# Performance work log

Hardware: AMD Instinct MI355X
Metric: run time of the kernel (lower is better)

## Reference

```python
import jax, jax.numpy as jnp
import numpy as np
import math

B, S, HID, NH = 4, 2048, 1024, 16
HD = HID // NH  # head dim = 64


def setup_inputs() -> dict:
    key = jax.random.key(0)
    ks = jax.random.split(key, 8)
    sc = 0.02
    return {
        "x": jax.random.normal(ks[0], (B, S, HID), dtype=jnp.float32),
        "att_mask": jnp.zeros((B, 1, 1, S), dtype=jnp.float32),
        "Wq": jax.random.normal(ks[1], (HID, HID), dtype=jnp.float32) * sc,
        "bq": jax.random.normal(ks[2], (HID,), dtype=jnp.float32) * sc,
        "Wk": jax.random.normal(ks[3], (HID, HID), dtype=jnp.float32) * sc,
        "bk": jax.random.normal(ks[4], (HID,), dtype=jnp.float32) * sc,
        "Wv": jax.random.normal(ks[5], (HID, HID), dtype=jnp.float32) * sc,
        "bv": jax.random.normal(ks[6], (HID,), dtype=jnp.float32) * sc,
    }


def reference(x, att_mask, Wq, bq, Wk, bk, Wv, bv):
    # quant_mode=False path: QuantLinear acts as a plain affine projection
    # (the running min/max stats only calibrate `scale`, which is unused in
    # the float path), and IntSoftmax reduces to a standard softmax.
    q = x @ Wq.T + bq  # [B,S,HID]
    k = x @ Wk.T + bk
    v = x @ Wv.T + bv
    # split heads: [B,S,HID] -> [B,NH,S,HD]
    q = q.reshape(B, S, NH, HD).transpose(0, 2, 1, 3)
    k = k.reshape(B, S, NH, HD).transpose(0, 2, 1, 3)
    v = v.reshape(B, S, NH, HD).transpose(0, 2, 1, 3)
    scores = jnp.einsum("bhqd,bhkd->bhqk", q, k) / math.sqrt(HD) + att_mask
    probs = jax.nn.softmax(scores, axis=-1)  # [B,NH,S,S]
    ctx = jnp.einsum("bhqk,bhkd->bhqd", probs, v)  # [B,NH,S,HD]
    return ctx.transpose(0, 2, 1, 3).reshape(B, S, HID)
```

## Files before the change

kernel.cpp:

```cpp
#include <hip/hip_runtime.h>
#include <hip/hip_bf16.h>
#include <cstdint>
#include <cstddef>

#define BB   4
#define SS   2048
#define HIDD 1024
#define NHH  16
#define HDD  64
#define MM   (BB*SS)
#define L2E  1.4426950408889634f
#define SH4  5.770780163555854f

typedef __bf16    bf16x8 __attribute__((ext_vector_type(8)));
typedef float     f32x4  __attribute__((ext_vector_type(4)));
typedef _Float16  half4  __attribute__((ext_vector_type(4)));
typedef _Float16  half8  __attribute__((ext_vector_type(8)));
typedef _Float16  half2v __attribute__((ext_vector_type(2)));

__device__ __forceinline__ unsigned short f2b(float f) {
    unsigned u = __builtin_bit_cast(unsigned, f);
    return (unsigned short)((u + 0x7FFFu + ((u >> 16) & 1u)) >> 16);
}

__device__ __forceinline__ half2v pkrtz(float a, float b) {
    return __builtin_bit_cast(half2v, __builtin_amdgcn_cvt_pkrtz(a, b));
}

__device__ __forceinline__ void gl_lds16(const void* g, void* l) {
    __builtin_amdgcn_global_load_lds(
        (const __attribute__((address_space(1))) void*)g,
        (__attribute__((address_space(3))) void*)l, 16, 0, 0);
}

#define NX4 (MM * HIDD / 4)
#define NW4 (HIDD * HIDD / 4)
__global__ __launch_bounds__(256) void cvt_all(
    const float* __restrict__ x,  const float* __restrict__ wq,
    const float* __restrict__ wk, const float* __restrict__ wv,
    unsigned short* __restrict__ xb, unsigned short* __restrict__ wb)
{
    int i = blockIdx.x * 256 + threadIdx.x;
    const float* src; unsigned short* dst; int off;
    if (i < NX4) { src = x; dst = xb; off = i; }
    else {
        int j = i - NX4;
        int w = j >> 18;
        off = j & (NW4 - 1);
        src = (w == 0) ? wq : (w == 1) ? wk : wv;
        dst = wb + (size_t)w * HIDD * HIDD;
    }
    float4 v = reinterpret_cast<const float4*>(src)[off];
    ushort4 o;
    o.x = f2b(v.x); o.y = f2b(v.y); o.z = f2b(v.z); o.w = f2b(v.w);
    reinterpret_cast<ushort4*>(dst)[off] = o;
}

__global__ __launch_bounds__(256, 3) void qkv_gemm(
    const unsigned short* __restrict__ xb,
    const unsigned short* __restrict__ wb,
    const float* __restrict__ bq, const float* __restrict__ bk, const float* __restrict__ bv,
    unsigned short* __restrict__ Qb, unsigned short* __restrict__ Kb,
    _Float16* __restrict__ Vtb)
{
    __shared__ unsigned short lA[128 * 64];
    __shared__ unsigned short lB[128 * 64];

    const int tid  = threadIdx.x;
    const int wave = tid >> 6, lane = tid & 63;
    const int lh   = lane & 15, quad = lane >> 4;
    const int l7   = lh & 7;
    const int m0   = blockIdx.x * 128;
    const int opn  = blockIdx.y;
    const int op   = opn >> 3;
    const int n0   = (opn & 7) * 128;
    const unsigned short* W = wb + (size_t)op * HIDD * HIDD;
    const float* bias = (op == 0) ? bq : (op == 1) ? bk : bv;

    f32x4 acc[4][4];
#pragma unroll
    for (int i = 0; i < 4; i++)
#pragma unroll
        for (int j = 0; j < 4; j++) acc[i][j] = f32x4{0.f, 0.f, 0.f, 0.f};

    const int wm = wave & 1, wn = wave >> 1;
    const unsigned short* srcA = (op == 2) ? lA : lB;
    const unsigned short* srcB = (op == 2) ? lB : lA;
    const int offA = (op == 2) ? wm : wn;
    const int offB = (op == 2) ? wn : wm;

    const int srow = tid >> 3;
    const int sg   = tid & 7;

    for (int k0 = 0; k0 < HIDD; k0 += 64) {
#pragma unroll
        for (int rr = 0; rr < 4; rr++) {
            const int row = srow + rr * 32;
            const int gcol = k0 + ((sg ^ (row & 7)) << 3);
            gl_lds16(&xb[(size_t)(m0 + row) * HIDD + gcol], &lA[row * 64 + sg * 8]);
            gl_lds16(&W [(size_t)(n0 + row) * HIDD + gcol], &lB[row * 64 + sg * 8]);
        }
        __syncthreads();

#pragma unroll
        for (int kk = 0; kk < 2; kk++) {
            bf16x8 aF[4], bF[4];
#pragma unroll
            for (int i = 0; i < 4; i++) {
                const int row = offA * 64 + i * 16 + lh;
                aF[i] = *reinterpret_cast<const bf16x8*>(
                    &srcA[row * 64 + (((kk * 4 + quad) ^ l7) << 3)]);
            }
#pragma unroll
            for (int j = 0; j < 4; j++) {
                const int row = offB * 64 + j * 16 + lh;
                bF[j] = *reinterpret_cast<const bf16x8*>(
                    &srcB[row * 64 + (((kk * 4 + quad) ^ l7) << 3)]);
            }
#pragma unroll
            for (int i = 0; i < 4; i++)
#pragma unroll
                for (int j = 0; j < 4; j++)
                    acc[i][j] = __builtin_amdgcn_mfma_f32_16x16x32_bf16(aF[i], bF[j], acc[i][j], 0, 0, 0);
        }
        __syncthreads();
    }

    if (op == 2) {
#pragma unroll
        for (int j = 0; j < 4; j++) {
            const int n = n0 + offB * 64 + j * 16 + lh;
            const float bvv = bias[n];
            const int h = n >> 6, d = n & 63;
#pragma unroll
            for (int i = 0; i < 4; i++) {
                const int mrow = m0 + offA * 64 + i * 16 + quad * 4;
                const int b_ = mrow >> 11, s_ = mrow & 2047;
                half2v h01 = pkrtz(acc[i][j][0] + bvv, acc[i][j][1] + bvv);
                half2v h23 = pkrtz(acc[i][j][2] + bvv, acc[i][j][3] + bvv);
                half4 hv; hv[0] = h01[0]; hv[1] = h01[1]; hv[2] = h23[0]; hv[3] = h23[1];
                size_t a = ((size_t)(b_ * NHH + h) * HDD + d) * SS + s_;
                *reinterpret_cast<half4*>(&Vtb[a]) = hv;
            }
        }
    } else {
        const float qs = (op == 0) ? (0.125f * L2E) : 1.0f;
        unsigned short* dst = (op == 0) ? Qb : Kb;
#pragma unroll
        for (int i = 0; i < 4; i++) {
            const int nb = n0 + offA * 64 + i * 16 + quad * 4;
            const float4 bb = *reinterpret_cast<const float4*>(&bias[nb]);
            const int h = nb >> 6, d = nb & 63;
#pragma unroll
            for (int j = 0; j < 4; j++) {
                const int m = m0 + offB * 64 + j * 16 + lh;
                const int b_ = m >> 11, s_ = m & 2047;
                ushort4 o;
                o.x = f2b((acc[i][j][0] + bb.x) * qs);
                o.y = f2b((acc[i][j][1] + bb.y) * qs);
                o.z = f2b((acc[i][j][2] + bb.z) * qs);
                o.w = f2b((acc[i][j][3] + bb.w) * qs);
                *reinterpret_cast<ushort4*>(
                    &dst[((size_t)(b_ * NHH + h) * SS + s_) * HDD + d]) = o;
            }
        }
    }
}

__global__ __launch_bounds__(256, 4) void attn_kernel(
    const unsigned short* __restrict__ Qb,
    const unsigned short* __restrict__ Kb,
    const _Float16* __restrict__ Vtb,
    const float* __restrict__ mask,
    float* __restrict__ out)
{
    __shared__ unsigned short lK[2][64 * 64];
    __shared__ _Float16      lV[2][64 * 64];

    const int tid  = threadIdx.x;
    const int wave = tid >> 6, lane = tid & 63;
    const int lh   = lane & 15, quad = lane >> 4;
    const int l7   = lh & 7;
    const int bh = blockIdx.x, qt = blockIdx.y;
    const int b = bh >> 4, h = bh & 15;
    const unsigned short* Qh = Qb  + (size_t)bh * SS * HDD;
    const unsigned short* Kh = Kb  + (size_t)bh * SS * HDD;
    const _Float16*       Vh = Vtb + (size_t)bh * HDD * SS;
    const float* mk = mask + (size_t)b * SS;
    const int q0 = qt * 128;

    bf16x8 qF[2][2];
#pragma unroll
    for (int i = 0; i < 2; i++)
#pragma unroll
        for (int kk = 0; kk < 2; kk++)
            qF[i][kk] = *reinterpret_cast<const bf16x8*>(
                &Qh[(size_t)(q0 + wave * 32 + i * 16 + lh) * HDD + kk * 32 + quad * 8]);

    f32x4 oacc[2][4];
#pragma unroll
    for (int i = 0; i < 2; i++)
#pragma unroll
        for (int dj = 0; dj < 4; dj++) oacc[i][dj] = f32x4{0.f, 0.f, 0.f, 0.f};
    float ls[2] = {0.f, 0.f};

    const int srow = tid >> 3;
    const int sg   = tid & 7;

#define STAGE(KT, BUF) do {                                                     \
    const int kb_ = (KT) * 64;                                                  \
    _Pragma("unroll")                                                           \
    for (int rr = 0; rr < 2; rr++) {                                            \
        const int row = srow + rr * 32;                                         \
        const int swk = ((sg ^ ((row & 3) | ((row >> 1) & 4))) << 3);           \
        const int swv = ((sg ^ (row & 7)) << 3);                                \
        gl_lds16(&Kh[(size_t)(kb_ + row) * HDD + swk], &lK[BUF][row * 64 + sg * 8]); \
        gl_lds16(&Vh[(size_t)row * SS + kb_ + swv],    &lV[BUF][row * 64 + sg * 8]); \
    }                                                                           \
} while (0)

    STAGE(0, 0);
    __syncthreads();

    for (int kt = 0; kt < SS / 64; kt++) {
        if (kt < SS / 64 - 1) STAGE(kt + 1, (kt + 1) & 1);
        const int buf = kt & 1;
        const int kb = kt * 64;

        float4 mg[4];
#pragma unroll
        for (int t = 0; t < 2; t++)
#pragma unroll
            for (int a = 0; a < 2; a++)
                mg[t * 2 + a] = *reinterpret_cast<const float4*>(
                    &mk[kb + t * 32 + quad * 8 + a * 4]);

        half8 pf[2][2];
#pragma unroll
        for (int t = 0; t < 2; t++) {
#pragma unroll
            for (int a = 0; a < 2; a++) {
                const int key = t * 32 + ((lh & 12) << 1) + (a << 2) + (lh & 3);
                const int krow = key * 64;
                bf16x8 kf0 = *reinterpret_cast<const bf16x8*>(
                    &lK[buf][krow + ((quad ^ l7) << 3)]);
                bf16x8 kf1 = *reinterpret_cast<const bf16x8*>(
                    &lK[buf][krow + (((4 + quad) ^ l7) << 3)]);
                const float4 m4 = mg[t * 2 + a];
                f32x4 mm;
                mm[0] = __builtin_fmaf(m4.x, L2E, -SH4);
                mm[1] = __builtin_fmaf(m4.y, L2E, -SH4);
                mm[2] = __builtin_fmaf(m4.z, L2E, -SH4);
                mm[3] = __builtin_fmaf(m4.w, L2E, -SH4);
#pragma unroll
                for (int i = 0; i < 2; i++) {
                    f32x4 s = __builtin_amdgcn_mfma_f32_16x16x32_bf16(kf0, qF[i][0], mm, 0, 0, 0);
                    s = __builtin_amdgcn_mfma_f32_16x16x32_bf16(kf1, qF[i][1], s, 0, 0, 0);
                    float e0 = __builtin_amdgcn_exp2f(s[0]);
                    float e1 = __builtin_amdgcn_exp2f(s[1]);
                    float e2 = __builtin_amdgcn_exp2f(s[2]);
                    float e3 = __builtin_amdgcn_exp2f(s[3]);
                    ls[i] += (e0 + e1) + (e2 + e3);
                    half2v p01 = pkrtz(e0, e1);
                    half2v p23 = pkrtz(e2, e3);
                    pf[t][i][a * 4 + 0] = p01[0];
                    pf[t][i][a * 4 + 1] = p01[1];
                    pf[t][i][a * 4 + 2] = p23[0];
                    pf[t][i][a * 4 + 3] = p23[1];
                }
            }
        }

#pragma unroll
        for (int t = 0; t < 2; t++) {
            half8 vf[4];
#pragma unroll
            for (int dj = 0; dj < 4; dj++)
                vf[dj] = *reinterpret_cast<const half8*>(
                    &lV[buf][(dj * 16 + lh) * 64 + (((t * 4 + quad) ^ l7) << 3)]);
#pragma unroll
            for (int i = 0; i < 2; i++)
#pragma unroll
                for (int dj = 0; dj < 4; dj++)
                    oacc[i][dj] = __builtin_amdgcn_mfma_f32_16x16x32_f16(
                        vf[dj], pf[t][i], oacc[i][dj], 0, 0, 0);
        }
        if (kt < SS / 64 - 1) __syncthreads();
    }

    float rls[2];
#pragma unroll
    for (int i = 0; i < 2; i++) {
        float l = ls[i];
        l += __shfl_xor(l, 16);
        l += __shfl_xor(l, 32);
        rls[i] = 1.0f / l;
    }
#pragma unroll
    for (int i = 0; i < 2; i++) {
        const int q = q0 + wave * 32 + i * 16 + lh;
#pragma unroll
        for (int dj = 0; dj < 4; dj++) {
            float4 o4;
            o4.x = oacc[i][dj][0] * rls[i];
            o4.y = oacc[i][dj][1] * rls[i];
            o4.z = oacc[i][dj][2] * rls[i];
            o4.w = oacc[i][dj][3] * rls[i];
            *reinterpret_cast<float4*>(
                &out[((size_t)b * SS + q) * HIDD + h * HDD + dj * 16 + quad * 4]) = o4;
        }
    }
}

extern "C" void kernel_launch(void* const* d_in, const int* in_sizes, int n_in,
                              void* d_out, int out_size, void* d_ws, size_t ws_size,
                              hipStream_t stream) {
    const float* x    = (const float*)d_in[0];
    const float* mask = (const float*)d_in[1];
    const float* Wq   = (const float*)d_in[2];
    const float* bq   = (const float*)d_in[3];
    const float* Wk   = (const float*)d_in[4];
    const float* bk   = (const float*)d_in[5];
    const float* Wv   = (const float*)d_in[6];
    const float* bv   = (const float*)d_in[7];
    float* out = (float*)d_out;
    (void)in_sizes; (void)n_in; (void)out_size; (void)ws_size;

    unsigned short* ws  = (unsigned short*)d_ws;
    unsigned short* xb  = ws;
    unsigned short* wb  = xb + (size_t)MM * HIDD;
    unsigned short* Qb  = wb + (size_t)3 * HIDD * HIDD;
    unsigned short* Kb  = Qb + (size_t)MM * HIDD;
    _Float16*       Vtb = (_Float16*)(Kb + (size_t)MM * HIDD);

    cvt_all<<<(NX4 + 3 * NW4) / 256, 256, 0, stream>>>(x, Wq, Wk, Wv, xb, wb);

    qkv_gemm<<<dim3(MM / 128, 24), 256, 0, stream>>>(xb, wb, bq, bk, bv, Qb, Kb, Vtb);

    attn_kernel<<<dim3(BB * NHH, SS / 128), 256, 0, stream>>>(Qb, Kb, Vtb, mask, out);
}
```

Before: 247.1 us.

## Compute softmax row sums via MFMA with ones vector, preload mask to LDS

The per-lane float adds and cross-lane shuffles that accumulated the softmax denominator are replaced by an extra MFMA against an all-ones f16 operand, so the row sum comes out of the matrix unit on the same fp16-rounded probabilities. The scaled additive mask is precomputed once per block into shared memory instead of being reloaded from global memory and rescaled each key tile. The PV section is also wrapped in s_setprio. This trades VALU work for one additional MFMA per 4 and adds 8KB of LDS per block, which may affect occupancy.

```diff
diff --git a/kernel.cpp b/kernel.cpp
--- a/kernel.cpp
+++ b/kernel.cpp
@@ -17,6 +17,7 @@
 typedef _Float16  half4  __attribute__((ext_vector_type(4)));
 typedef _Float16  half8  __attribute__((ext_vector_type(8)));
 typedef _Float16  half2v __attribute__((ext_vector_type(2)));
+typedef unsigned  u32x4  __attribute__((ext_vector_type(4)));
 
 __device__ __forceinline__ unsigned short f2b(float f) {
     unsigned u = __builtin_bit_cast(unsigned, f);
@@ -25,6 +26,10 @@
 
 __device__ __forceinline__ half2v pkrtz(float a, float b) {
     return __builtin_bit_cast(half2v, __builtin_amdgcn_cvt_pkrtz(a, b));
+}
+
+__device__ __forceinline__ unsigned pkrtz_u(float a, float b) {
+    return __builtin_bit_cast(unsigned, __builtin_amdgcn_cvt_pkrtz(a, b));
 }
 
 __device__ __forceinline__ void gl_lds16(const void* g, void* l) {
@@ -176,6 +181,7 @@
 {
     __shared__ unsigned short lK[2][64 * 64];
     __shared__ _Float16      lV[2][64 * 64];
+    __shared__ float         lmm[SS];
 
     const int tid  = threadIdx.x;
     const int wave = tid >> 6, lane = tid & 63;
@@ -202,7 +208,10 @@
     for (int i = 0; i < 2; i++)
 #pragma unroll
         for (int dj = 0; dj < 4; dj++) oacc[i][dj] = f32x4{0.f, 0.f, 0.f, 0.f};
-    float ls[2] = {0.f, 0.f};
+    f32x4 osum[2] = {f32x4{0.f, 0.f, 0.f, 0.f}, f32x4{0.f, 0.f, 0.f, 0.f}};
+
+    const u32x4 one_u = {0x3C003C00u, 0x3C003C00u, 0x3C003C00u, 0x3C003C00u};
+    const half8 vone  = __builtin_bit_cast(half8, one_u);
 
     const int srow = tid >> 3;
     const int sg   = tid & 7;
@@ -220,6 +229,18 @@
 } while (0)
 
     STAGE(0, 0);
+
+#pragma unroll
+    for (int j = 0; j < 2; j++) {
+        const int idx = tid * 8 + j * 4;
+        float4 m = *reinterpret_cast<const float4*>(&mk[idx]);
+        float4 r;
+        r.x = __builtin_fmaf(m.x, L2E, -SH4);
+        r.y = __builtin_fmaf(m.y, L2E, -SH4);
+        r.z = __builtin_fmaf(m.z, L2E, -SH4);
+        r.w = __builtin_fmaf(m.w, L2E, -SH4);
+        *reinterpret_cast<float4*>(&lmm[idx]) = r;
+    }
     __syncthreads();
 
     for (int kt = 0; kt < SS / 64; kt++) {
@@ -227,15 +248,7 @@
         const int buf = kt & 1;
         const int kb = kt * 64;
 
-        float4 mg[4];
-#pragma unroll
-        for (int t = 0; t < 2; t++)
-#pragma unroll
-            for (int a = 0; a < 2; a++)
-                mg[t * 2 + a] = *reinterpret_cast<const float4*>(
-                    &mk[kb + t * 32 + quad * 8 + a * 4]);
-
-        half8 pf[2][2];
+        unsigned pw[2][2][4];
 #pragma unroll
         for (int t = 0; t < 2; t++) {
 #pragma unroll
@@ -246,31 +259,21 @@
                     &lK[buf][krow + ((quad ^ l7) << 3)]);
                 bf16x8 kf1 = *reinterpret_cast<const bf16x8*>(
                     &lK[buf][krow + (((4 + quad) ^ l7) << 3)]);
-                const float4 m4 = mg[t * 2 + a];
-                f32x4 mm;
-                mm[0] = __builtin_fmaf(m4.x, L2E, -SH4);
-                mm[1] = __builtin_fmaf(m4.y, L2E, -SH4);
-                mm[2] = __builtin_fmaf(m4.z, L2E, -SH4);
-                mm[3] = __builtin_fmaf(m4.w, L2E, -SH4);
+                const f32x4 mm = *reinterpret_cast<const f32x4*>(
+                    &lmm[kb + t * 32 + quad * 8 + a * 4]);
 #pragma unroll
                 for (int i = 0; i < 2; i++) {
                     f32x4 s = __builtin_amdgcn_mfma_f32_16x16x32_bf16(kf0, qF[i][0], mm, 0, 0, 0);
                     s = __builtin_amdgcn_mfma_f32_16x16x32_bf16(kf1, qF[i][1], s, 0, 0, 0);
-                    float e0 = __builtin_amdgcn_exp2f(s[0]);
-                    float e1 = __builtin_amdgcn_exp2f(s[1]);
-                    float e2 = __builtin_amdgcn_exp2f(s[2]);
-                    float e3 = __builtin_amdgcn_exp2f(s[3]);
-                    ls[i] += (e0 + e1) + (e2 + e3);
-                    half2v p01 = pkrtz(e0, e1);
-                    half2v p23 = pkrtz(e2, e3);
-                    pf[t][i][a * 4 + 0] = p01[0];
-                    pf[t][i][a * 4 + 1] = p01[1];
-                    pf[t][i][a * 4 + 2] = p23[0];
-                    pf[t][i][a * 4 + 3] = p23[1];
+                    pw[t][i][a * 2 + 0] = pkrtz_u(__builtin_amdgcn_exp2f(s[0]),
+                                                  __builtin_amdgcn_exp2f(s[1]));
+                    pw[t][i][a * 2 + 1] = pkrtz_u(__builtin_amdgcn_exp2f(s[2]),
+                                                  __builtin_amdgcn_exp2f(s[3]));
                 }
             }
         }
 
+        __builtin_amdgcn_s_setprio(1);
 #pragma unroll
         for (int t = 0; t < 2; t++) {
             half8 vf[4];
@@ -279,33 +282,31 @@
                 vf[dj] = *reinterpret_cast<const half8*>(
                     &lV[buf][(dj * 16 + lh) * 64 + (((t * 4 + quad) ^ l7) << 3)]);
 #pragma unroll
-            for (int i = 0; i < 2; i++)
+            for (int i = 0; i < 2; i++) {
+                const u32x4 pu = {pw[t][i][0], pw[t][i][1], pw[t][i][2], pw[t][i][3]};
+                const half8 pF = __builtin_bit_cast(half8, pu);
+                osum[i] = __builtin_amdgcn_mfma_f32_16x16x32_f16(vone, pF, osum[i], 0, 0, 0);
 #pragma unroll
                 for (int dj = 0; dj < 4; dj++)
                     oacc[i][dj] = __builtin_amdgcn_mfma_f32_16x16x32_f16(
-                        vf[dj], pf[t][i], oacc[i][dj], 0, 0, 0);
-        }
+                        vf[dj], pF, oacc[i][dj], 0, 0, 0);
+            }
+        }
+        __builtin_amdgcn_s_setprio(0);
         if (kt < SS / 64 - 1) __syncthreads();
     }
 
-    float rls[2];
 #pragma unroll
     for (int i = 0; i < 2; i++) {
-        float l = ls[i];
-        l += __shfl_xor(l, 16);
-        l += __shfl_xor(l, 32);
-        rls[i] = 1.0f / l;
-    }
-#pragma unroll
-    for (int i = 0; i < 2; i++) {
+        const float rls = 1.0f / osum[i][0];
         const int q = q0 + wave * 32 + i * 16 + lh;
 #pragma unroll
         for (int dj = 0; dj < 4; dj++) {
             float4 o4;
-            o4.x = oacc[i][dj][0] * rls[i];
-            o4.y = oacc[i][dj][1] * rls[i];
-            o4.z = oacc[i][dj][2] * rls[i];
-            o4.w = oacc[i][dj][3] * rls[i];
+            o4.x = oacc[i][dj][0] * rls;
+            o4.y = oacc[i][dj][1] * rls;
+            o4.z = oacc[i][dj][2] * rls;
+            o4.w = oacc[i][dj][3] * rls;
             *reinterpret_cast<float4*>(
                 &out[((size_t)b * SS + q) * HIDD + h * HDD + dj * 16 + quad * 4]) = o4;
         }
```

Result: faster. 236.2 us (-4.4%).
